# Performance work log

Measured on AMD Instinct MI355X. Metric: run time of the kernel, lower is better.

Reference implementation:

```python
import jax, jax.numpy as jnp
import numpy as np

DIM = 768
NUM_HEADS = 12
HEAD_DIM = DIM // NUM_HEADS
H = W = 64
RANK = 4
LORA_SCALING = 1.0 / RANK  # lora_alpha(=1) / r


def setup_inputs() -> dict:
    key = jax.random.key(0)
    ks = jax.random.split(key, 11)
    s = 0.02
    return {
        "x": jax.random.normal(ks[0], (1, H, W, DIM), dtype=jnp.float32),
        "W_qkv": jax.random.normal(ks[1], (3 * DIM, DIM), dtype=jnp.float32) * s,
        "b_qkv": jax.random.normal(ks[2], (3 * DIM,), dtype=jnp.float32) * s,
        "A_q": jax.random.normal(ks[3], (RANK, DIM), dtype=jnp.float32) * s,
        "B_q": jax.random.normal(ks[4], (DIM, RANK), dtype=jnp.float32) * s,
        "A_v": jax.random.normal(ks[5], (RANK, DIM), dtype=jnp.float32) * s,
        "B_v": jax.random.normal(ks[6], (DIM, RANK), dtype=jnp.float32) * s,
        "rel_h": jax.random.normal(ks[7], (2 * H - 1, HEAD_DIM), dtype=jnp.float32) * s,
        "rel_w": jax.random.normal(ks[8], (2 * W - 1, HEAD_DIM), dtype=jnp.float32) * s,
        "W_proj": jax.random.normal(ks[9], (DIM, DIM), dtype=jnp.float32) * s,
        "b_proj": jax.random.normal(ks[10], (DIM,), dtype=jnp.float32) * s,
    }


def _get_rel_pos(size, rel_pos):
    # q_size == k_size == size; relative coords indexed into (2*size-1, head_dim)
    coords = jnp.arange(size)[:, None] - jnp.arange(size)[None, :] + (size - 1)
    return rel_pos[coords]  # (size, size, head_dim)


def reference(x, W_qkv, b_qkv, A_q, B_q, A_v, B_v, rel_h, rel_w, W_proj, b_proj):
    B, h, w, dim = x.shape
    nh, hd = NUM_HEADS, HEAD_DIM
    scale = hd ** -0.5
    n = h * w
    xf = x.reshape(B, n, dim)

    # LoRA-merged QKV: base linear + low-rank deltas on q and v thirds only
    qkv = xf @ W_qkv.T + b_qkv  # (B, n, 3*dim)
    dq = ((xf @ A_q.T) @ B_q.T) * LORA_SCALING
    dv = ((xf @ A_v.T) @ B_v.T) * LORA_SCALING
    qkv = qkv.at[..., :dim].add(dq).at[..., 2 * dim:].add(dv)

    qkv = qkv.reshape(B, n, 3, nh, hd).transpose(2, 0, 3, 1, 4).reshape(3, B * nh, n, hd)
    q, k, v = qkv[0], qkv[1], qkv[2]  # each (B*nh, n, hd)

    attn = (q * scale) @ jnp.swapaxes(k, -2, -1)  # (B*nh, n, n)

    # decomposed relative position bias (SAM style)
    Rh = _get_rel_pos(h, rel_h)  # (h, h, hd)
    Rw = _get_rel_pos(w, rel_w)  # (w, w, hd)
    r_q = q.reshape(B * nh, h, w, hd)
    bias_h = jnp.einsum("bhwc,hkc->bhwk", r_q, Rh)  # (B*nh, h, w, h)
    bias_w = jnp.einsum("bhwc,wkc->bhwk", r_q, Rw)  # (B*nh, h, w, w)
    attn = (attn.reshape(B * nh, h, w, h, w)
            + bias_h[:, :, :, :, None]
            + bias_w[:, :, :, None, :]).reshape(B * nh, n, n)

    attn = jax.nn.softmax(attn, axis=-1)
    out = (attn @ v).reshape(B, nh, h, w, hd).transpose(0, 2, 3, 1, 4).reshape(B, h, w, dim)
    return out @ W_proj.T + b_proj
```

## Files before the change

### kernel.cpp

```cpp
#include <hip/hip_runtime.h>

#define NTOK 4096
#define DIMD 768
#define NHD  12
#define HDD  64
#define DK   800

typedef float  f32x2  __attribute__((ext_vector_type(2)));
typedef float  f32x4  __attribute__((ext_vector_type(4)));
typedef float  f32x16 __attribute__((ext_vector_type(16)));
typedef short  s16x8  __attribute__((ext_vector_type(8)));

#define MFMA16(a, b, c) __builtin_amdgcn_mfma_f32_16x16x32_bf16(a, b, c, 0, 0, 0)
#define MFMA32(a, b, c) __builtin_amdgcn_mfma_f32_32x32x16_bf16(a, b, c, 0, 0, 0)

#if __has_builtin(__builtin_amdgcn_exp2f)
#define EXP2(x) __builtin_amdgcn_exp2f(x)
#else
#define EXP2(x) exp2f(x)
#endif

__device__ inline short f2b(float f) {
  unsigned u = __float_as_uint(f);
  u += 0x7FFFu + ((u >> 16) & 1u);
  return (short)(u >> 16);
}
__device__ inline float b2f(short s) {
  return __uint_as_float(((unsigned)(unsigned short)s) << 16);
}
__device__ inline void gl_lds16(const short* g, short* l) {
  __builtin_amdgcn_global_load_lds(
      (const __attribute__((address_space(1))) unsigned int*)g,
      (__attribute__((address_space(3))) unsigned int*)l, 16, 0, 0);
}


__global__ __launch_bounds__(64)
void k_prep_w(const float* __restrict__ Wqkv, const float* __restrict__ Bq,
              const float* __restrict__ Bv, const float* __restrict__ Wp,
              short* __restrict__ we, short* __restrict__ wpb) {
  const int j = blockIdx.x;
  const int l = threadIdx.x;
  if (j < 2304) {
#pragma unroll
    for (int k = 0; k < 12; ++k)
      we[(size_t)j * DK + l + 64 * k] = f2b(Wqkv[(size_t)j * DIMD + l + 64 * k]);
    if (l < 32) {
      int c = 768 + l;
      short v = 0;
      if (l < 4) {
        if (j < 768) v = f2b(Bq[j * 4 + l]);
      } else if (l < 8) {
        if (j >= 1536) v = f2b(Bv[(j - 1536) * 4 + (l - 4)]);
      }
      we[(size_t)j * DK + c] = v;
    }
  } else {
    const int jr = j - 2304;
#pragma unroll
    for (int k = 0; k < 12; ++k)
      wpb[(size_t)jr * DIMD + l + 64 * k] =
          f2b(Wp[(size_t)jr * DIMD + l + 64 * k]);
  }
}

__global__ __launch_bounds__(64)
void k_prep_x(const float* __restrict__ x, const float* __restrict__ Aq,
              const float* __restrict__ Av, short* __restrict__ xe) {
  const int i = blockIdx.x;
  const int l = threadIdx.x;
  float xv[12];
#pragma unroll
  for (int k = 0; k < 12; ++k) xv[k] = x[(size_t)i * DIMD + l + 64 * k];
#pragma unroll
  for (int k = 0; k < 12; ++k)
    xe[(size_t)i * DK + l + 64 * k] = f2b(xv[k]);
  float a8[8];
#pragma unroll
  for (int o = 0; o < 8; ++o) {
    const float* A = (o < 4) ? (Aq + o * DIMD) : (Av + (o - 4) * DIMD);
    float acc = 0.f;
#pragma unroll
    for (int k = 0; k < 12; ++k) acc = fmaf(xv[k], A[l + 64 * k], acc);
#pragma unroll
    for (int off = 32; off; off >>= 1) acc += __shfl_xor(acc, off, 64);
    a8[o] = acc;
  }
  if (l < 32) {
    float v = 0.f;
#pragma unroll
    for (int o = 0; o < 8; ++o)
      if (l == o) v = 0.25f * a8[o];
    xe[(size_t)i * DK + 768 + l] = (l < 8) ? f2b(v) : (short)0;
  }
}

__global__ __launch_bounds__(256)
void k_qkv(const short* __restrict__ xe, const short* __restrict__ we,
           const float* __restrict__ bqkv, short* __restrict__ qkvb,
           short* __restrict__ vtb) {
  const int d_ = blockIdx.y * 18 + blockIdx.x;
  const int lin = (d_ & 7) * 72 + (d_ >> 3);
  const int j0 = (lin % 18) * 128;
  const int i0 = (lin / 18) * 128;

  __shared__ __align__(16) short shm[16640];
  short* As = shm;
  short* Bs = shm + 8192;
  short* Cs = shm;

  const int t = threadIdx.x, lane = t & 63, w = t >> 6;
  const int l15 = lane & 15, quad = lane >> 4;
  const int wm = w >> 1, wn = w & 1;

  f32x4 acc[4][4];
#pragma unroll
  for (int a = 0; a < 4; ++a)
#pragma unroll
    for (int b = 0; b < 4; ++b) acc[a][b] = (f32x4){0.f, 0.f, 0.f, 0.f};

  for (int kk = 0; kk < 768; kk += 64) {
    __syncthreads();
#pragma unroll
    for (int rep = 0; rep < 4; ++rep) {
      int c = rep * 256 + w * 64 + lane;
      int row = c >> 3, u = (c & 7) ^ (row & 7);
      gl_lds16(xe + (size_t)(i0 + row) * DK + kk + u * 8,
               &As[(rep * 256 + w * 64) * 8]);
      gl_lds16(we + (size_t)(j0 + row) * DK + kk + u * 8,
               &Bs[(rep * 256 + w * 64) * 8]);
    }
    __syncthreads();
#pragma unroll
    for (int kh2 = 0; kh2 < 2; ++kh2) {
      s16x8 af[4], bf[4];
#pragma unroll
      for (int mt = 0; mt < 4; ++mt) {
        int row = wm * 64 + mt * 16 + l15;
        af[mt] = *(const s16x8*)&As[row * 64 +
                                    (((kh2 * 4 + quad) ^ (l15 & 7)) * 8)];
      }
#pragma unroll
      for (int nt = 0; nt < 4; ++nt) {
        int row = wn * 64 + nt * 16 + l15;
        bf[nt] = *(const s16x8*)&Bs[row * 64 +
                                    (((kh2 * 4 + quad) ^ (l15 & 7)) * 8)];
      }
#pragma unroll
      for (int mt = 0; mt < 4; ++mt)
#pragma unroll
        for (int nt = 0; nt < 4; ++nt)
          acc[mt][nt] = MFMA16(af[mt], bf[nt], acc[mt][nt]);
    }
  }

  __syncthreads();
#pragma unroll
  for (int rep = 0; rep < 2; ++rep) {
    int c = rep * 256 + w * 64 + lane;
    gl_lds16(xe + (size_t)(i0 + (c >> 2)) * DK + 768 + (c & 3) * 8,
             &As[(rep * 256 + w * 64) * 8]);
    gl_lds16(we + (size_t)(j0 + (c >> 2)) * DK + 768 + (c & 3) * 8,
             &Bs[(rep * 256 + w * 64) * 8]);
  }
  __syncthreads();
  {
    s16x8 af[4], bf[4];
#pragma unroll
    for (int mt = 0; mt < 4; ++mt)
      af[mt] = *(const s16x8*)&As[(wm * 64 + mt * 16 + l15) * 32 + quad * 8];
#pragma unroll
    for (int nt = 0; nt < 4; ++nt)
      bf[nt] = *(const s16x8*)&Bs[(wn * 64 + nt * 16 + l15) * 32 + quad * 8];
#pragma unroll
    for (int mt = 0; mt < 4; ++mt)
#pragma unroll
      for (int nt = 0; nt < 4; ++nt)
        acc[mt][nt] = MFMA16(af[mt], bf[nt], acc[mt][nt]);
  }
  __syncthreads();

  const int which = j0 / DIMD;
  float bj[4];
#pragma unroll
  for (int nt = 0; nt < 4; ++nt) bj[nt] = bqkv[j0 + wn * 64 + nt * 16 + l15];

#pragma unroll
  for (int mt = 0; mt < 4; ++mt)
#pragma unroll
    for (int r = 0; r < 4; ++r) {
      const int row = wm * 64 + mt * 16 + quad * 4 + r;
#pragma unroll
      for (int nt = 0; nt < 4; ++nt) {
        const int col = wn * 64 + nt * 16 + l15;
        Cs[row * 130 + col] = f2b(acc[mt][nt][r] + bj[nt]);
      }
    }
  __syncthreads();
  const int base_head = (j0 - which * DIMD) >> 6;
  if (which != 2) {
#pragma unroll
    for (int rp = 0; rp < 8; ++rp) {
      int f = t + 256 * rp;
      int row = f >> 4, ch = f & 15;
      int head = base_head + (ch >> 3);
      int ddb = (ch & 7) * 8;
      s16x8 v = *(const s16x8*)&Cs[row * 130 + ch * 8];
      *(s16x8*)&qkvb[(((size_t)which * NHD + head) * NTOK + i0 + row) * HDD + ddb] = v;
    }
  } else {
#pragma unroll
    for (int rp = 0; rp < 8; ++rp) {
      int f = t + 256 * rp;
      int dcol = f >> 4, n8 = (f & 15) * 8;
      unsigned wds[4];
#pragma unroll
      for (int m = 0; m < 4; ++m) {
        int s0 = n8 + 2 * m, s1 = s0 + 1;
        int sr0 = (s0 & 0x70) | ((((s0 >> 2) & 3) == 1 ? 2 : ((s0 >> 2) & 3) == 2 ? 1 : ((s0 >> 2) & 3)) << 2) | (s0 & 3);
        int sr1 = (s1 & 0x70) | ((((s1 >> 2) & 3) == 1 ? 2 : ((s1 >> 2) & 3) == 2 ? 1 : ((s1 >> 2) & 3)) << 2) | (s1 & 3);
        unsigned lo = (unsigned short)Cs[sr0 * 130 + dcol];
        unsigned hi = (unsigned short)Cs[sr1 * 130 + dcol];
        wds[m] = lo | (hi << 16);
      }
      short* dst = vtb + ((size_t)(base_head * 64) + dcol) * NTOK + i0 + n8;
      *(int4*)dst = *(int4*)&wds[0];
    }
  }
}

__global__ __launch_bounds__(256)
void k_attn7(const short* __restrict__ qkvb, const short* __restrict__ vtb,
             const float* __restrict__ relh, const float* __restrict__ relw,
             short* __restrict__ attnb) {
  const int d_ = blockIdx.y * 64 + blockIdx.x;
  const int lin = (d_ & 7) * 96 + (d_ >> 3);
  const int head = lin >> 6;
  const int hq = lin & 63;
  const int n0 = hq * 64;

  __shared__ short sm[20480];
  short* smb = sm;

  const short* qg  = qkvb + (size_t)(0 * NHD + head) * NTOK * HDD;
  const short* kg  = qkvb + (size_t)(1 * NHD + head) * NTOK * HDD;
  const short* vtg = vtb + (size_t)head * HDD * NTOK;

  const int t = threadIdx.x;
  const int w = t >> 6, lane = t & 63;
  const int l31 = lane & 31, h = lane >> 5;
  const int kh = w >> 1, qh = w & 1;
  const int q = qh * 32 + l31;

  const int rowp = lane >> 1;
  const int cw = (w * 2 + (lane & 1)) * 8;
  const short* gK0 = kg + (size_t)rowp * HDD + cw;
  const short* gK1 = gK0 + 32 * HDD;
  const short* gV0 = vtg + (size_t)rowp * NTOK + cw;
  const short* gV1 = gV0 + (size_t)32 * NTOK;

  s16x8 qb[4];
#pragma unroll
  for (int s = 0; s < 4; ++s)
    qb[s] = *(const s16x8*)&qg[(size_t)(n0 + q) * HDD + s * 16 + 8 * h];

#pragma unroll
  for (int rp = 0; rp < 4; ++rp) {
    int f = t + 256 * rp;
    int d = f >> 3, c = (f & 7) * 8;
    float4 v0 = make_float4(0, 0, 0, 0), v1 = v0;
    if (d < 127) {
      const float* s_ = relw + (size_t)d * HDD + c;
      v0 = *(const float4*)s_; v1 = *(const float4*)(s_ + 4);
    }
    short4 b0, b1;
    b0.x = f2b(v0.x); b0.y = f2b(v0.y); b0.z = f2b(v0.z); b0.w = f2b(v0.w);
    b1.x = f2b(v1.x); b1.y = f2b(v1.y); b1.z = f2b(v1.z); b1.w = f2b(v1.w);
    *(short4*)&smb[d * 72 + c] = b0;
    *(short4*)&smb[d * 72 + c + 4] = b1;
  }
  __syncthreads();

  f32x16 mc0 = (f32x16)(0.f), mc1 = (f32x16)(0.f);
#pragma unroll
  for (int s = 0; s < 4; ++s) {
    s16x8 a0 = *(const s16x8*)&smb[((kh * 2) * 32 + l31) * 72 + s * 16 + 8 * h];
    s16x8 a1 = *(const s16x8*)&smb[((kh * 2 + 1) * 32 + l31) * 72 + s * 16 + 8 * h];
    mc0 = MFMA32(a0, qb[s], mc0);
    mc1 = MFMA32(a1, qb[s], mc1);
  }
  __syncthreads();
#pragma unroll
  for (int reg = 0; reg < 16; ++reg) {
    int dl = (reg & 3) + 8 * (reg >> 2) + 4 * h;
    smb[(kh * 64 + dl) * 64 + q] = f2b(mc0[reg] * 1.44269504f);
    smb[(kh * 64 + 32 + dl) * 64 + q] = f2b(mc1[reg] * 1.44269504f);
  }
  __syncthreads();

  f32x2 bw2[8];
#pragma unroll
  for (int i = 0; i < 8; ++i)
#pragma unroll
    for (int p = 0; p < 2; ++p) {
      int reg = 2 * i + p;
      int kl64 = kh * 32 + (reg & 3) + 8 * (reg >> 2) + 4 * h;
      int dneed = q - kl64 + 63;
      bw2[i][p] = b2f(smb[dneed * 64 + q]);
    }
  __syncthreads();

#pragma unroll
  for (int rp = 0; rp < 2; ++rp) {
    int f = t + 256 * rp;
    int kt = f >> 3, c = (f & 7) * 8;
    const float* s_ = relh + (size_t)(hq + 63 - kt) * HDD + c;
    float4 v0 = *(const float4*)s_, v1 = *(const float4*)(s_ + 4);
    short4 b0, b1;
    b0.x = f2b(v0.x); b0.y = f2b(v0.y); b0.z = f2b(v0.z); b0.w = f2b(v0.w);
    b1.x = f2b(v1.x); b1.y = f2b(v1.y); b1.z = f2b(v1.z); b1.w = f2b(v1.w);
    *(short4*)&smb[kt * 72 + c] = b0;
    *(short4*)&smb[kt * 72 + c + 4] = b1;
  }
  __syncthreads();

  f32x16 hc = (f32x16)(0.f);
#pragma unroll
  for (int s = 0; s < 4; ++s) {
    s16x8 a = *(const s16x8*)&smb[(kh * 32 + l31) * 72 + s * 16 + 8 * h];
    hc = MFMA32(a, qb[s], hc);
  }
#pragma unroll
  for (int reg = 0; reg < 16; ++reg) {
    int ktl = kh * 32 + (reg & 3) + 8 * (reg >> 2) + 4 * h;
    smb[16384 + ktl * 64 + q] = f2b(hc[reg] * 1.44269504f);
  }
  __syncthreads();

  gl_lds16(gK0, smb + 0 + w * 512);
  gl_lds16(gK1, smb + 2048 + w * 512);
  gK0 += 4096; gK1 += 4096;
  gl_lds16(gV0, smb + 8192 + w * 512);
  gl_lds16(gV1, smb + 8192 + 2048 + w * 512);
  gV0 += 64; gV1 += 64;
  gl_lds16(gK0, smb + 4096 + w * 512);
  gl_lds16(gK1, smb + 4096 + 2048 + w * 512);
  gK0 += 4096; gK1 += 4096;

  int baseS[4], baseV[2];
#pragma unroll
  for (int s = 0; s < 4; ++s)
    baseS[s] = kh * 2048 + s * 512 + l31 * 16 + h * 8;
#pragma unroll
  for (int s2 = 0; s2 < 2; ++s2)
    baseV[s2] = (kh * 2 + s2) * 512 + l31 * 16 + h * 8;

  f32x2 ps2 = (f32x2)(0.f);
  f32x16 oc0 = (f32x16)(0.f), oc1 = (f32x16)(0.f);
  unsigned pkA[8], pkB[8];

  __syncthreads();

  {
    f32x16 sc_ = (f32x16)(0.f);
#pragma unroll
    for (int s = 0; s < 4; ++s) {
      s16x8 a = *(const s16x8*)&smb[0 + baseS[s]];
      sc_ = MFMA32(a, qb[s], sc_);
    }
    float bhl2 = b2f(smb[16384 + 0 * 64 + q]);
#pragma unroll
    for (int i = 0; i < 8; ++i) {
      f32x2 s2;
      s2[0] = sc_[2 * i]; s2[1] = sc_[2 * i + 1];
      f32x2 r = s2 * 0.18033688f + (bw2[i] + bhl2);
      float e0 = EXP2(r[0]);
      float e1 = EXP2(r[1]);
      f32x2 e2; e2[0] = e0; e2[1] = e1;
      ps2 += e2;
      pkA[i] = __builtin_amdgcn_perm(__float_as_uint(e1),
                                     __float_as_uint(e0), 0x07060302u);
    }
  }

#define ITER_P(KTN, VOFF, KOFFN, KDST, VDST, PFK, PFV, PKC, PKN)               \
  {                                                                            \
    __syncthreads();                                                           \
    if (PFK) {                                                                 \
      gl_lds16(gK0, smb + (KDST) + w * 512);                                   \
      gl_lds16(gK1, smb + (KDST) + 2048 + w * 512);                            \
      gK0 += 4096; gK1 += 4096;                                                \
    }                                                                          \
    if (PFV) {                                                                 \
      gl_lds16(gV0, smb + (VDST) + w * 512);                                   \
      gl_lds16(gV1, smb + (VDST) + 2048 + w * 512);                            \
      gV0 += 64; gV1 += 64;                                                    \
    }                                                                          \
    f32x16 sc_ = (f32x16)(0.f);                                                \
    _Pragma("unroll") for (int s = 0; s < 4; ++s) {                            \
      s16x8 a = *(const s16x8*)&smb[(KOFFN) + baseS[s]];                       \
      sc_ = MFMA32(a, qb[s], sc_);                                             \
    }                                                                          \
    _Pragma("unroll") for (int s2i = 0; s2i < 2; ++s2i) {                      \
      union { unsigned u[4]; s16x8 v; } B;                                     \
      B.u[0] = PKC[4 * s2i + 0];                                               \
      B.u[1] = PKC[4 * s2i + 1];                                               \
      B.u[2] = PKC[4 * s2i + 2];                                               \
      B.u[3] = PKC[4 * s2i + 3];                                               \
      s16x8 a0 = *(const s16x8*)&smb[(VOFF) + baseV[s2i]];                     \
      s16x8 a1 = *(const s16x8*)&smb[(VOFF) + 2048 + baseV[s2i]];              \
      oc0 = MFMA32(a0, B.v, oc0);                                              \
      oc1 = MFMA32(a1, B.v, oc1);                                              \
    }                                                                          \
    float bhl2 = b2f(smb[16384 + (KTN) * 64 + q]);                             \
    _Pragma("unroll") for (int i = 0; i < 8; ++i) {                            \
      f32x2 s2;                                                                \
      s2[0] = sc_[2 * i]; s2[1] = sc_[2 * i + 1];                              \
      f32x2 r = s2 * 0.18033688f + (bw2[i] + bhl2);                            \
      float e0 = EXP2(r[0]);                                                   \
      float e1 = EXP2(r[1]);                                                   \
      f32x2 e2; e2[0] = e0; e2[1] = e1;                                        \
      ps2 += e2;                                                               \
      PKN[i] = __builtin_amdgcn_perm(__float_as_uint(e1),                      \
                                     __float_as_uint(e0), 0x07060302u);        \
    }                                                                          \
  }

  for (int m = 0; m < 31; ++m) {
    ITER_P(2 * m + 1, 8192, 4096, 0, 12288, 1, 1, pkA, pkB);
    ITER_P(2 * m + 2, 12288, 0, 4096, 8192, 1, 1, pkB, pkA);
  }
  ITER_P(63, 8192, 4096, 0, 12288, 0, 1, pkA, pkB);
  __syncthreads();
#pragma unroll
  for (int s2i = 0; s2i < 2; ++s2i) {
    union { unsigned u[4]; s16x8 v; } B;
    B.u[0] = pkB[4 * s2i + 0];
    B.u[1] = pkB[4 * s2i + 1];
    B.u[2] = pkB[4 * s2i + 2];
    B.u[3] = pkB[4 * s2i + 3];
    s16x8 a0 = *(const s16x8*)&smb[12288 + baseV[s2i]];
    s16x8 a1 = *(const s16x8*)&smb[12288 + 2048 + baseV[s2i]];
    oc0 = MFMA32(a0, B.v, oc0);
    oc1 = MFMA32(a1, B.v, oc1);
  }
#undef ITER_P

  __syncthreads();
  float ps = ps2[0] + ps2[1];
  float* obuf = (float*)smb;
  float* psb  = (float*)smb + 4224;
  short* tbuf = smb + 8576;
  ps += __shfl_xor(ps, 32, 64);
  if (kh == 1) {
#pragma unroll
    for (int reg = 0; reg < 16; ++reg) {
      int dl = (reg & 3) + 8 * (reg >> 2) + 4 * h;
      obuf[dl * 66 + q] = oc0[reg];
      obuf[(32 + dl) * 66 + q] = oc1[reg];
    }
    if (lane < 32) psb[q] = ps;
  }
  __syncthreads();
  if (kh == 0) {
    float inv = 1.f / (ps + psb[q]);
#pragma unroll
    for (int reg = 0; reg < 16; ++reg) {
      int dl = (reg & 3) + 8 * (reg >> 2) + 4 * h;
      tbuf[dl * 66 + q] = f2b((oc0[reg] + obuf[dl * 66 + q]) * inv);
      tbuf[(32 + dl) * 66 + q] = f2b((oc1[reg] + obuf[(32 + dl) * 66 + q]) * inv);
    }
  }
  __syncthreads();
  {
    int qq = t >> 2, seg = t & 3;
    unsigned wds[8];
#pragma unroll
    for (int m = 0; m < 8; ++m) {
      unsigned lo = (unsigned short)tbuf[(seg * 16 + 2 * m) * 66 + qq];
      unsigned hi = (unsigned short)tbuf[(seg * 16 + 2 * m + 1) * 66 + qq];
      wds[m] = lo | (hi << 16);
    }
    short* dst = attnb + (size_t)(n0 + qq) * DIMD + head * 64 + seg * 16;
    *(int4*)dst = *(int4*)&wds[0];
    *(int4*)(dst + 8) = *(int4*)&wds[4];
  }
}

__global__ __launch_bounds__(256)
void k_proj(const short* __restrict__ ab, const short* __restrict__ wpb,
            const float* __restrict__ bp, float* __restrict__ out) {
  const int d_ = blockIdx.y * 12 + blockIdx.x;
  const int lin = (d_ & 7) * 48 + (d_ >> 3);
  const int j0 = (lin % 12) * 64;
  const int i0 = (lin / 12) * 128;
  __shared__ short As[128 * 32];
  __shared__ short Bs[64 * 32];
  const int t = threadIdx.x, lane = t & 63, w = t >> 6;
  const int l15 = lane & 15, quad = lane >> 4;
  const int wm = w >> 1, wn = w & 1;

  f32x4 acc[4][2];
#pragma unroll
  for (int a = 0; a < 4; ++a)
#pragma unroll
    for (int b = 0; b < 2; ++b) acc[a][b] = (f32x4){0.f, 0.f, 0.f, 0.f};

  for (int kk = 0; kk < DIMD; kk += 32) {
    __syncthreads();
#pragma unroll
    for (int rep = 0; rep < 2; ++rep) {
      int c = rep * 256 + w * 64 + lane;
      gl_lds16(ab + (size_t)(i0 + (c >> 2)) * DIMD + kk + (c & 3) * 8,
               &As[(rep * 256 + w * 64) * 8]);
    }
    {
      gl_lds16(wpb + (size_t)(j0 + ((w * 64 + lane) >> 2)) * DIMD + kk +
                   ((w * 64 + lane) & 3) * 8,
               &Bs[(w * 64) * 8]);
    }
    __syncthreads();
    s16x8 af[4], bf[2];
#pragma unroll
    for (int mt = 0; mt < 4; ++mt)
      af[mt] = *(const s16x8*)&As[(wm * 64 + mt * 16 + l15) * 32 + quad * 8];
#pragma unroll
    for (int nt = 0; nt < 2; ++nt)
      bf[nt] = *(const s16x8*)&Bs[(wn * 32 + nt * 16 + l15) * 32 + quad * 8];
#pragma unroll
    for (int mt = 0; mt < 4; ++mt)
#pragma unroll
      for (int nt = 0; nt < 2; ++nt)
        acc[mt][nt] = MFMA16(af[mt], bf[nt], acc[mt][nt]);
  }

#pragma unroll
  for (int mt = 0; mt < 4; ++mt)
#pragma unroll
    for (int r = 0; r < 4; ++r) {
      const int i = i0 + wm * 64 + mt * 16 + quad * 4 + r;
#pragma unroll
      for (int nt = 0; nt < 2; ++nt) {
        const int j = j0 + wn * 32 + nt * 16 + l15;
        out[(size_t)i * DIMD + j] = acc[mt][nt][r] + bp[j];
      }
    }
}

extern "C" void kernel_launch(void* const* d_in, const int* in_sizes, int n_in,
                              void* d_out, int out_size, void* d_ws, size_t ws_size,
                              hipStream_t stream) {
  (void)in_sizes; (void)n_in; (void)out_size; (void)ws_size;
  const float* x    = (const float*)d_in[0];
  const float* Wqkv = (const float*)d_in[1];
  const float* bqkv = (const float*)d_in[2];
  const float* Aq   = (const float*)d_in[3];
  const float* Bq   = (const float*)d_in[4];
  const float* Av   = (const float*)d_in[5];
  const float* Bv   = (const float*)d_in[6];
  const float* relh = (const float*)d_in[7];
  const float* relw = (const float*)d_in[8];
  const float* Wp   = (const float*)d_in[9];
  const float* bp   = (const float*)d_in[10];
  float* out = (float*)d_out;

  float* ws = (float*)d_ws;
  short* xe    = (short*)(ws);
  short* we    = (short*)(ws + 1638400);
  short* wpb   = (short*)(ws + 2560000);
  short* qkvb  = (short*)(ws + 2854912);
  short* vtb   = (short*)(ws + 7573504);
  short* attnb = (short*)(ws + 9146368);

  k_prep_w<<<dim3(3072), dim3(64), 0, stream>>>(Wqkv, Bq, Bv, Wp, we, wpb);
  k_prep_x<<<dim3(NTOK), dim3(64), 0, stream>>>(x, Aq, Av, xe);
  k_qkv<<<dim3(18, 32), dim3(256), 0, stream>>>(xe, we, bqkv, qkvb, vtb);
  k_attn7<<<dim3(64, NHD), dim3(256), 0, stream>>>(qkvb, vtb, relh, relw, attnb);
  k_proj<<<dim3(12, 32), dim3(256), 0, stream>>>(attnb, wpb, bp, out);
}
```

Baseline: 224.0 us.

## Process two key tiles per iteration with explicit waitcnt and barrier scheduling

Restructures the attention main loop to load and compute two K tiles and two V tiles per step instead of a one-tile-ahead software pipeline. It uses explicit s_waitcnt and s_barrier with sched_barrier fences, so global-to-LDS prefetches are issued right after the QK MFMAs finish reading the buffers. The aim is fewer barriers per tile and larger batches of independent MFMA work. The cost is less overlap between loads and compute, because K and V now reuse the same buffers and must wait for the previous readers.

```diff
diff --git a/kernel.cpp b/kernel.cpp
--- a/kernel.cpp
+++ b/kernel.cpp
@@ -339,13 +339,14 @@
 
   gl_lds16(gK0, smb + 0 + w * 512);
   gl_lds16(gK1, smb + 2048 + w * 512);
-  gK0 += 4096; gK1 += 4096;
+  gl_lds16(gK0 + 4096, smb + 4096 + w * 512);
+  gl_lds16(gK1 + 4096, smb + 4096 + 2048 + w * 512);
+  gK0 += 8192; gK1 += 8192;
   gl_lds16(gV0, smb + 8192 + w * 512);
   gl_lds16(gV1, smb + 8192 + 2048 + w * 512);
-  gV0 += 64; gV1 += 64;
-  gl_lds16(gK0, smb + 4096 + w * 512);
-  gl_lds16(gK1, smb + 4096 + 2048 + w * 512);
-  gK0 += 4096; gK1 += 4096;
+  gl_lds16(gV0 + 64, smb + 12288 + w * 512);
+  gl_lds16(gV1 + 64, smb + 12288 + 2048 + w * 512);
+  gV0 += 128; gV1 += 128;
 
   int baseS[4], baseV[2];
 #pragma unroll
@@ -357,94 +358,83 @@
 
   f32x2 ps2 = (f32x2)(0.f);
   f32x16 oc0 = (f32x16)(0.f), oc1 = (f32x16)(0.f);
-  unsigned pkA[8], pkB[8];
-
-  __syncthreads();
-
-  {
-    f32x16 sc_ = (f32x16)(0.f);
-#pragma unroll
-    for (int s = 0; s < 4; ++s) {
-      s16x8 a = *(const s16x8*)&smb[0 + baseS[s]];
-      sc_ = MFMA32(a, qb[s], sc_);
-    }
-    float bhl2 = b2f(smb[16384 + 0 * 64 + q]);
-#pragma unroll
-    for (int i = 0; i < 8; ++i) {
-      f32x2 s2;
-      s2[0] = sc_[2 * i]; s2[1] = sc_[2 * i + 1];
-      f32x2 r = s2 * 0.18033688f + (bw2[i] + bhl2);
-      float e0 = EXP2(r[0]);
-      float e1 = EXP2(r[1]);
-      f32x2 e2; e2[0] = e0; e2[1] = e1;
-      ps2 += e2;
-      pkA[i] = __builtin_amdgcn_perm(__float_as_uint(e1),
-                                     __float_as_uint(e0), 0x07060302u);
-    }
-  }
-
-#define ITER_P(KTN, VOFF, KOFFN, KDST, VDST, PFK, PFV, PKC, PKN)               \
-  {                                                                            \
-    __syncthreads();                                                           \
-    if (PFK) {                                                                 \
-      gl_lds16(gK0, smb + (KDST) + w * 512);                                   \
-      gl_lds16(gK1, smb + (KDST) + 2048 + w * 512);                            \
-      gK0 += 4096; gK1 += 4096;                                                \
-    }                                                                          \
-    if (PFV) {                                                                 \
-      gl_lds16(gV0, smb + (VDST) + w * 512);                                   \
-      gl_lds16(gV1, smb + (VDST) + 2048 + w * 512);                            \
-      gV0 += 64; gV1 += 64;                                                    \
-    }                                                                          \
-    f32x16 sc_ = (f32x16)(0.f);                                                \
-    _Pragma("unroll") for (int s = 0; s < 4; ++s) {                            \
-      s16x8 a = *(const s16x8*)&smb[(KOFFN) + baseS[s]];                       \
-      sc_ = MFMA32(a, qb[s], sc_);                                             \
-    }                                                                          \
+
+#define SM_BLOCK(SC, BHL, PK)                                                  \
+    _Pragma("unroll") for (int i = 0; i < 8; ++i) {                            \
+      f32x2 s2;                                                                \
+      s2[0] = (SC)[2 * i]; s2[1] = (SC)[2 * i + 1];                            \
+      f32x2 r = s2 * 0.18033688f + (bw2[i] + (BHL));                           \
+      float e0 = EXP2(r[0]);                                                   \
+      float e1 = EXP2(r[1]);                                                   \
+      f32x2 e2; e2[0] = e0; e2[1] = e1;                                        \
+      ps2 += e2;                                                               \
+      PK[i] = __builtin_amdgcn_perm(__float_as_uint(e1),                       \
+                                    __float_as_uint(e0), 0x07060302u);         \
+    }
+
+#define PV_BLOCK(VOFF, PK)                                                     \
     _Pragma("unroll") for (int s2i = 0; s2i < 2; ++s2i) {                      \
       union { unsigned u[4]; s16x8 v; } B;                                     \
-      B.u[0] = PKC[4 * s2i + 0];                                               \
-      B.u[1] = PKC[4 * s2i + 1];                                               \
-      B.u[2] = PKC[4 * s2i + 2];                                               \
-      B.u[3] = PKC[4 * s2i + 3];                                               \
+      B.u[0] = PK[4 * s2i + 0]; B.u[1] = PK[4 * s2i + 1];                      \
+      B.u[2] = PK[4 * s2i + 2]; B.u[3] = PK[4 * s2i + 3];                      \
       s16x8 a0 = *(const s16x8*)&smb[(VOFF) + baseV[s2i]];                     \
       s16x8 a1 = *(const s16x8*)&smb[(VOFF) + 2048 + baseV[s2i]];              \
       oc0 = MFMA32(a0, B.v, oc0);                                              \
       oc1 = MFMA32(a1, B.v, oc1);                                              \
+    }
+
+#define ITER2(KTa, PF)                                                         \
+  {                                                                            \
+    asm volatile("s_waitcnt vmcnt(4)" ::: "memory");                           \
+    __builtin_amdgcn_s_barrier();                                              \
+    __builtin_amdgcn_sched_barrier(0);                                         \
+    f32x16 sa = (f32x16)(0.f), sb = (f32x16)(0.f);                             \
+    _Pragma("unroll") for (int s = 0; s < 4; ++s) {                            \
+      s16x8 ka = *(const s16x8*)&smb[0 + baseS[s]];                            \
+      sa = MFMA32(ka, qb[s], sa);                                              \
     }                                                                          \
-    float bhl2 = b2f(smb[16384 + (KTN) * 64 + q]);                             \
-    _Pragma("unroll") for (int i = 0; i < 8; ++i) {                            \
-      f32x2 s2;                                                                \
-      s2[0] = sc_[2 * i]; s2[1] = sc_[2 * i + 1];                              \
-      f32x2 r = s2 * 0.18033688f + (bw2[i] + bhl2);                            \
-      float e0 = EXP2(r[0]);                                                   \
-      float e1 = EXP2(r[1]);                                                   \
-      f32x2 e2; e2[0] = e0; e2[1] = e1;                                        \
-      ps2 += e2;                                                               \
-      PKN[i] = __builtin_amdgcn_perm(__float_as_uint(e1),                      \
-                                     __float_as_uint(e0), 0x07060302u);        \
+    _Pragma("unroll") for (int s = 0; s < 4; ++s) {                            \
+      s16x8 kb = *(const s16x8*)&smb[4096 + baseS[s]];                         \
+      sb = MFMA32(kb, qb[s], sb);                                              \
     }                                                                          \
-  }
-
-  for (int m = 0; m < 31; ++m) {
-    ITER_P(2 * m + 1, 8192, 4096, 0, 12288, 1, 1, pkA, pkB);
-    ITER_P(2 * m + 2, 12288, 0, 4096, 8192, 1, 1, pkB, pkA);
-  }
-  ITER_P(63, 8192, 4096, 0, 12288, 0, 1, pkA, pkB);
-  __syncthreads();
-#pragma unroll
-  for (int s2i = 0; s2i < 2; ++s2i) {
-    union { unsigned u[4]; s16x8 v; } B;
-    B.u[0] = pkB[4 * s2i + 0];
-    B.u[1] = pkB[4 * s2i + 1];
-    B.u[2] = pkB[4 * s2i + 2];
-    B.u[3] = pkB[4 * s2i + 3];
-    s16x8 a0 = *(const s16x8*)&smb[12288 + baseV[s2i]];
-    s16x8 a1 = *(const s16x8*)&smb[12288 + 2048 + baseV[s2i]];
-    oc0 = MFMA32(a0, B.v, oc0);
-    oc1 = MFMA32(a1, B.v, oc1);
-  }
-#undef ITER_P
+    float bhla = b2f(smb[16384 + (KTa) * 64 + q]);                             \
+    float bhlb = b2f(smb[16384 + (KTa) * 64 + 64 + q]);                        \
+    asm volatile("s_waitcnt lgkmcnt(0) vmcnt(0)" ::: "memory");                \
+    __builtin_amdgcn_sched_barrier(0);                                         \
+    __builtin_amdgcn_s_barrier();                                              \
+    __builtin_amdgcn_sched_barrier(0);                                         \
+    if (PF) {                                                                  \
+      gl_lds16(gK0, smb + 0 + w * 512);                                        \
+      gl_lds16(gK1, smb + 2048 + w * 512);                                     \
+      gl_lds16(gK0 + 4096, smb + 4096 + w * 512);                              \
+      gl_lds16(gK1 + 4096, smb + 4096 + 2048 + w * 512);                       \
+      gK0 += 8192; gK1 += 8192;                                                \
+    }                                                                          \
+    unsigned pkA[8], pkB[8];                                                   \
+    SM_BLOCK(sa, bhla, pkA);                                                   \
+    PV_BLOCK(8192, pkA);                                                       \
+    SM_BLOCK(sb, bhlb, pkB);                                                   \
+    PV_BLOCK(12288, pkB);                                                      \
+    if (PF) {                                                                  \
+      asm volatile("s_waitcnt lgkmcnt(0)" ::: "memory");                       \
+      __builtin_amdgcn_sched_barrier(0);                                       \
+      __builtin_amdgcn_s_barrier();                                            \
+      __builtin_amdgcn_sched_barrier(0);                                       \
+      gl_lds16(gV0, smb + 8192 + w * 512);                                     \
+      gl_lds16(gV1, smb + 8192 + 2048 + w * 512);                              \
+      gl_lds16(gV0 + 64, smb + 12288 + w * 512);                               \
+      gl_lds16(gV1 + 64, smb + 12288 + 2048 + w * 512);                        \
+      gV0 += 128; gV1 += 128;                                                  \
+    }                                                                          \
+  }
+
+  for (int t2 = 0; t2 < 31; ++t2) {
+    ITER2(2 * t2, 1);
+  }
+  ITER2(62, 0);
+#undef ITER2
+#undef SM_BLOCK
+#undef PV_BLOCK
 
   __syncthreads();
   float ps = ps2[0] + ps2[1];
```

Result: no change. 222.1 us (-0.8%).
